# Kernel optimization log

Hardware: AMD Instinct MI355X
Metric: run time of the kernel (lower is better)

## Reference

```python
import jax, jax.numpy as jnp
import numpy as np

NUM_HEADS = 16


def setup_inputs() -> dict:
    key = jax.random.key(0)
    k1, k2, k3 = jax.random.split(key, 3)
    B, N, C = 2, 2048, 1024
    x = jax.random.normal(k1, (B, N, C), dtype=jnp.float32)
    w_qkv = jax.random.normal(k2, (3 * C, C), dtype=jnp.float32) * (C ** -0.5)
    w_proj = jax.random.normal(k3, (C, C), dtype=jnp.float32) * (C ** -0.5)
    b_proj = jnp.zeros((C,), dtype=jnp.float32)
    return {"x": x, "w_qkv": w_qkv, "w_proj": w_proj, "b_proj": b_proj}


def reference(x, w_qkv, w_proj, b_proj):
    B, N, C = x.shape
    H = NUM_HEADS
    D = C // H
    scale = 1.0 / jnp.sqrt(jnp.asarray(D, x.dtype))
    qkv = (x @ w_qkv.T).reshape(B, N, 3, H, D)
    qkv = jnp.transpose(qkv, (2, 0, 3, 1, 4))  # [3,B,H,N,D]
    q, k, v = qkv[0], qkv[1], qkv[2]
    # scaled dot-product attention with explicit score matrix [B,H,N,N]
    attn = jnp.einsum('bhnd,bhmd->bhnm', q, k) * scale
    attn = jax.nn.softmax(attn, axis=-1)
    out = jnp.einsum('bhnm,bhmd->bhnd', attn, v)
    out = jnp.transpose(out, (0, 2, 1, 3)).reshape(B, N, C)
    # output projection
    return out @ w_proj.T + b_proj
```

## Files before the change

kernel.cpp:

```cpp
#include <hip/hip_runtime.h>

typedef unsigned short u16;
typedef __attribute__((ext_vector_type(8))) short bf16x8;
typedef __attribute__((ext_vector_type(4))) float f32x4;
typedef __attribute__((ext_vector_type(16))) float f32x16;
typedef __attribute__((ext_vector_type(4))) unsigned u32x4;

#define B_ 2
#define N_ 2048
#define C_ 1024
#define H_ 16
#define D_ 64
#define M_ (B_ * N_)

#define QSCALE 0.18033688011114336f

#define EXP2R(x) __builtin_amdgcn_exp2f(x)

__device__ __forceinline__ u16 f2bf(float f) {
    union { float f; unsigned u; } x; x.f = f;
    return (u16)((x.u + 0x8000u) >> 16);
}
__device__ __forceinline__ unsigned pack2bf(float a, float b) {
    union { float f; unsigned u; } x, y; x.f = a; y.f = b;
    return __builtin_amdgcn_perm(y.u + 0x8000u, x.u + 0x8000u, 0x07060302);
}

__device__ __forceinline__ void async_copy16(const void* gsrc, void* ldst) {
    __builtin_amdgcn_global_load_lds(
        (__attribute__((address_space(1))) void*)gsrc,
        (__attribute__((address_space(3))) void*)ldst,
        16, 0, 0);
}

__global__ void cast3_kernel(const float* __restrict__ x, const float* __restrict__ wq,
                             const float* __restrict__ wp, u16* __restrict__ xo,
                             u16* __restrict__ wqo, u16* __restrict__ wpo) {
    int b = blockIdx.x;
    const float* s; u16* d;
    if (b < 4096)      { s = x;  d = xo;  }
    else if (b < 7168) { s = wq; d = wqo; b -= 4096; }
    else               { s = wp; d = wpo; b -= 7168; }
    int i = (b * 256 + threadIdx.x) * 4;
    const float4 v = *(const float4*)(s + i);
    uint2 o;
    o.x = pack2bf(v.x, v.y);
    o.y = pack2bf(v.z, v.w);
    *(uint2*)(d + i) = o;
}

template <int EPI>
__global__ __launch_bounds__(256, 3) void gemm_bt(
    const u16* __restrict__ A, const u16* __restrict__ Bm,
    int M, int Ncols, int K, int ntiles_n,
    u16* __restrict__ qo, u16* __restrict__ ko, u16* __restrict__ vt,
    const float* __restrict__ bias, float* __restrict__ out) {
    __shared__ u16 As[128 * 64];
    __shared__ u16 Bs[128 * 64];
    const int tid = threadIdx.x, lane = tid & 63, w = tid >> 6;
    const int cpx = gridDim.x >> 3;
    const int sbid = (blockIdx.x & 7) * cpx + (blockIdx.x >> 3);
    const int bx = sbid % ntiles_n, by = sbid / ntiles_n;
    const int m0 = by * 128, n0 = bx * 128;
    const int wm = w >> 1, wn = w & 1;
    const int q16 = lane >> 4, l15 = lane & 15;
    const int r0 = lane >> 3, c0 = (lane & 7) * 8;
    f32x4 acc[4][4] = {};

    for (int k0 = 0; k0 < K; k0 += 64) {
#pragma unroll
        for (int i = 0; i < 4; ++i) {
            int blk = w * 4 + i;
            int r = blk * 8 + r0;
            async_copy16(A + (size_t)(m0 + r) * K + k0 + c0, (char*)As + blk * 1024);
            async_copy16(Bm + (size_t)(n0 + r) * K + k0 + c0, (char*)Bs + blk * 1024);
        }
        __builtin_amdgcn_s_waitcnt(0);
        __syncthreads();
#pragma unroll
        for (int ks = 0; ks < 2; ++ks) {
            bf16x8 af[4], bf[4];
#pragma unroll
            for (int i = 0; i < 4; ++i) {
                af[i] = *(const bf16x8*)&As[(wm * 64 + i * 16 + l15) * 64 + ks * 32 + q16 * 8];
                bf[i] = *(const bf16x8*)&Bs[(wn * 64 + i * 16 + l15) * 64 + ks * 32 + q16 * 8];
            }
#pragma unroll
            for (int mi = 0; mi < 4; ++mi)
#pragma unroll
                for (int ni = 0; ni < 4; ++ni)
                    acc[mi][ni] = __builtin_amdgcn_mfma_f32_16x16x32_bf16(af[mi], bf[ni], acc[mi][ni], 0, 0, 0);
        }
        __syncthreads();
    }

#pragma unroll
    for (int mi = 0; mi < 4; ++mi) {
#pragma unroll
        for (int ni = 0; ni < 4; ++ni) {
            int n_g = n0 + wn * 64 + ni * 16 + l15;
            if (EPI == 0) {
                int which = n_g >> 10;
                int h = (n_g >> 6) & 15;
                int d = n_g & 63;
                int m_base = m0 + wm * 64 + mi * 16 + q16 * 4;
                int b = m_base >> 11;
                int nn0 = m_base & 2047;
                if (which == 2) {
                    uint2 pk;
                    pk.x = pack2bf(acc[mi][ni][0], acc[mi][ni][1]);
                    pk.y = pack2bf(acc[mi][ni][2], acc[mi][ni][3]);
                    *(uint2*)(vt + ((size_t)((b * H_ + h) * D_ + d) << 11) + nn0) = pk;
                } else {
                    size_t base = ((size_t)((b * H_ + h) * N_ + nn0) << 6) + d;
#pragma unroll
                    for (int r = 0; r < 4; ++r) {
                        float v = acc[mi][ni][r];
                        if (which == 0) qo[base + (size_t)r * D_] = f2bf(v * QSCALE);
                        else            ko[base + (size_t)r * D_] = f2bf(v);
                    }
                }
            } else {
#pragma unroll
                for (int r = 0; r < 4; ++r) {
                    int m_g = m0 + wm * 64 + mi * 16 + q16 * 4 + r;
                    out[(size_t)m_g * Ncols + n_g] = acc[mi][ni][r] + bias[n_g];
                }
            }
        }
    }
}

__global__ __launch_bounds__(512, 1) void attn_kernel(
    const u16* __restrict__ Q, const u16* __restrict__ K,
    const u16* __restrict__ VT, u16* __restrict__ O) {
    __shared__ u16 Ks[2][2][64 * 64];
    __shared__ u16 Vs[2][2][64 * 64];
    const int tid = threadIdx.x, lane = tid & 63, w = tid >> 6;
    const int l31 = lane & 31, hi = lane >> 5, l7 = l31 & 7;
    const int bid = blockIdx.x;
    const int bh = (bid & 7) * 4 + (bid >> 6);
    const int q0 = ((bid >> 3) & 7) * 256;
    const size_t head = (size_t)bh * N_ * D_;
    const int lr3 = lane >> 3, lc7 = lane & 7;

    auto stage = [&](int kt, int buf) {
        int key0 = kt * 128;
        int row = w * 8 + lr3;
#pragma unroll
        for (int s = 0; s < 2; ++s) {
            async_copy16(K + head + (size_t)(key0 + s * 64 + row) * D_ + (lc7 ^ lr3) * 8,
                         (char*)Ks[buf][s] + w * 1024);
            async_copy16(VT + head + (size_t)row * N_ + key0 + s * 64 + (lc7 ^ lr3) * 8,
                         (char*)Vs[buf][s] + w * 1024);
        }
    };

    bf16x8 qf[4];
#pragma unroll
    for (int ds = 0; ds < 4; ++ds)
        qf[ds] = *(const bf16x8*)(Q + head + (size_t)(q0 + w * 32 + l31) * D_ + ds * 16 + hi * 8);
    stage(0, 0);
    __builtin_amdgcn_s_waitcnt(0);
    __syncthreads();

    f32x16 o_acc[2] = {};
    float rs = 0.f;

    for (int kt = 0; kt < 16; ++kt) {
        int buf = kt & 1;
        stage((kt + 1) & 15, buf ^ 1);

#pragma unroll
        for (int s = 0; s < 2; ++s) {
#pragma unroll
            for (int kb2 = 0; kb2 < 2; ++kb2) {
                f32x16 st = {};
                __builtin_amdgcn_s_setprio(1);
#pragma unroll
                for (int ds = 0; ds < 4; ++ds) {
                    bf16x8 kf = *(const bf16x8*)&Ks[buf][s][(kb2 * 32 + l31) * 64 + ((ds * 2 + hi) ^ l7) * 8];
                    st = __builtin_amdgcn_mfma_f32_32x32x16_bf16(kf, qf[ds], st, 0, 0, 0);
                }
                __builtin_amdgcn_s_setprio(0);

                float p[16];
#pragma unroll
                for (int i = 0; i < 16; ++i) p[i] = EXP2R(st[i]);
#pragma unroll
                for (int i = 0; i < 16; ++i) rs += p[i];

                unsigned a0 = pack2bf(p[0], p[1]),   b0 = pack2bf(p[4], p[5]);
                unsigned a1 = pack2bf(p[2], p[3]),   b1 = pack2bf(p[6], p[7]);
                unsigned a2 = pack2bf(p[8], p[9]),   b2 = pack2bf(p[12], p[13]);
                unsigned a3 = pack2bf(p[10], p[11]), b3 = pack2bf(p[14], p[15]);
                asm("v_permlane32_swap_b32 %0, %1" : "+v"(a0), "+v"(b0));
                asm("v_permlane32_swap_b32 %0, %1" : "+v"(a1), "+v"(b1));
                asm("v_permlane32_swap_b32 %0, %1" : "+v"(a2), "+v"(b2));
                asm("v_permlane32_swap_b32 %0, %1" : "+v"(a3), "+v"(b3));
                union { u32x4 u; bf16x8 v; } af0, af1;
                af0.u = (u32x4){a0, a1, b0, b1};
                af1.u = (u32x4){a2, a3, b2, b3};

                __builtin_amdgcn_s_setprio(1);
#pragma unroll
                for (int db = 0; db < 2; ++db) {
                    bf16x8 vf0 = *(const bf16x8*)&Vs[buf][s][(db * 32 + l31) * 64 + ((kb2 * 4 + hi) ^ l7) * 8];
                    o_acc[db] = __builtin_amdgcn_mfma_f32_32x32x16_bf16(af0.v, vf0, o_acc[db], 0, 0, 0);
                    bf16x8 vf1 = *(const bf16x8*)&Vs[buf][s][(db * 32 + l31) * 64 + ((kb2 * 4 + 2 + hi) ^ l7) * 8];
                    o_acc[db] = __builtin_amdgcn_mfma_f32_32x32x16_bf16(af1.v, vf1, o_acc[db], 0, 0, 0);
                }
                __builtin_amdgcn_s_setprio(0);
            }
        }

        __builtin_amdgcn_s_waitcnt(0);
        __syncthreads();
    }

    rs += __shfl_xor(rs, 32);
    float rsi = 1.0f / rs;

    const int b = bh >> 4, h = bh & 15;
#pragma unroll
    for (int reg = 0; reg < 16; ++reg) {
        int qrow = (reg & 3) + 8 * (reg >> 2) + 4 * hi;
        float inv = __shfl(rsi, qrow);
        int qg = q0 + w * 32 + qrow;
#pragma unroll
        for (int db = 0; db < 2; ++db) {
            int d = db * 32 + l31;
            O[((size_t)(b * N_ + qg) << 10) + h * 64 + d] = f2bf(o_acc[db][reg] * inv);
        }
    }
}

extern "C" void kernel_launch(void* const* d_in, const int* in_sizes, int n_in,
                              void* d_out, int out_size, void* d_ws, size_t ws_size,
                              hipStream_t stream) {
    const float* x      = (const float*)d_in[0];
    const float* w_qkv  = (const float*)d_in[1];
    const float* w_proj = (const float*)d_in[2];
    const float* b_proj = (const float*)d_in[3];
    float* out = (float*)d_out;

    char* ws = (char*)d_ws;
    const size_t MB = 1024 * 1024;
    u16* x_bf     = (u16*)(ws + 0 * MB);
    u16* wqkv_bf  = (u16*)(ws + 8 * MB);
    u16* wproj_bf = (u16*)(ws + 14 * MB);
    u16* q_bf     = (u16*)(ws + 16 * MB);
    u16* k_bf     = (u16*)(ws + 24 * MB);
    u16* vt_bf    = (u16*)(ws + 32 * MB);
    u16* ao_bf    = (u16*)(ws + 40 * MB);

    cast3_kernel<<<8192, 256, 0, stream>>>(x, w_qkv, w_proj, x_bf, wqkv_bf, wproj_bf);

    gemm_bt<0><<<32 * 24, 256, 0, stream>>>(x_bf, wqkv_bf, M_, 3 * C_, C_, 24,
                                            q_bf, k_bf, vt_bf, nullptr, nullptr);

    attn_kernel<<<256, 512, 0, stream>>>(q_bf, k_bf, vt_bf, ao_bf);

    gemm_bt<1><<<32 * 8, 256, 0, stream>>>(ao_bf, wproj_bf, M_, C_, C_, 8,
                                           nullptr, nullptr, nullptr, b_proj, out);
}
```

Baseline: 181.7 us.

## Process two query tiles per wave in attention, halving waves per block

The attention kernel now runs 4 waves per block instead of 8. Each wave handles 64 query rows split into two 32-row groups, so every K and V fragment read from LDS feeds two MFMAs instead of one. The staging loop gives each wave twice as many async copies so the same tile is still loaded. The bf16 packing of probabilities also switches to the hardware v_cvt_pk_bf16_f32 instruction. In exchange, register pressure roughly doubles and fewer waves per CU are available to hide latency.

```diff
diff --git a/kernel.cpp b/kernel.cpp
--- a/kernel.cpp
+++ b/kernel.cpp
@@ -24,6 +24,11 @@
 __device__ __forceinline__ unsigned pack2bf(float a, float b) {
     union { float f; unsigned u; } x, y; x.f = a; y.f = b;
     return __builtin_amdgcn_perm(y.u + 0x8000u, x.u + 0x8000u, 0x07060302);
+}
+__device__ __forceinline__ unsigned cvtpk2bf(float a, float b) {
+    unsigned r;
+    asm("v_cvt_pk_bf16_f32 %0, %1, %2" : "=v"(r) : "v"(a), "v"(b));
+    return r;
 }
 
 __device__ __forceinline__ void async_copy16(const void* gsrc, void* ldst) {
@@ -131,7 +136,7 @@
     }
 }
 
-__global__ __launch_bounds__(512, 1) void attn_kernel(
+__global__ __launch_bounds__(256, 1) void attn_kernel(
     const u16* __restrict__ Q, const u16* __restrict__ K,
     const u16* __restrict__ VT, u16* __restrict__ O) {
     __shared__ u16 Ks[2][2][64 * 64];
@@ -146,26 +151,32 @@
 
     auto stage = [&](int kt, int buf) {
         int key0 = kt * 128;
-        int row = w * 8 + lr3;
-#pragma unroll
-        for (int s = 0; s < 2; ++s) {
-            async_copy16(K + head + (size_t)(key0 + s * 64 + row) * D_ + (lc7 ^ lr3) * 8,
-                         (char*)Ks[buf][s] + w * 1024);
-            async_copy16(VT + head + (size_t)row * N_ + key0 + s * 64 + (lc7 ^ lr3) * 8,
-                         (char*)Vs[buf][s] + w * 1024);
-        }
+#pragma unroll
+        for (int s = 0; s < 2; ++s)
+#pragma unroll
+            for (int i = 0; i < 2; ++i) {
+                int c = w * 2 + i;
+                int row = c * 8 + lr3;
+                async_copy16(K + head + (size_t)(key0 + s * 64 + row) * D_ + (lc7 ^ lr3) * 8,
+                             (char*)Ks[buf][s] + c * 1024);
+                async_copy16(VT + head + (size_t)row * N_ + key0 + s * 64 + (lc7 ^ lr3) * 8,
+                             (char*)Vs[buf][s] + c * 1024);
+            }
     };
 
-    bf16x8 qf[4];
-#pragma unroll
-    for (int ds = 0; ds < 4; ++ds)
-        qf[ds] = *(const bf16x8*)(Q + head + (size_t)(q0 + w * 32 + l31) * D_ + ds * 16 + hi * 8);
+    bf16x8 qf[2][4];
+#pragma unroll
+    for (int qg = 0; qg < 2; ++qg)
+#pragma unroll
+        for (int ds = 0; ds < 4; ++ds)
+            qf[qg][ds] = *(const bf16x8*)(Q + head +
+                (size_t)(q0 + w * 64 + qg * 32 + l31) * D_ + ds * 16 + hi * 8);
     stage(0, 0);
     __builtin_amdgcn_s_waitcnt(0);
     __syncthreads();
 
-    f32x16 o_acc[2] = {};
-    float rs = 0.f;
+    f32x16 o_acc[2][2] = {};
+    float rs[2] = {0.f, 0.f};
 
     for (int kt = 0; kt < 16; ++kt) {
         int buf = kt & 1;
@@ -175,40 +186,49 @@
         for (int s = 0; s < 2; ++s) {
 #pragma unroll
             for (int kb2 = 0; kb2 < 2; ++kb2) {
-                f32x16 st = {};
+                bf16x8 kf[4];
+#pragma unroll
+                for (int ds = 0; ds < 4; ++ds)
+                    kf[ds] = *(const bf16x8*)&Ks[buf][s][(kb2 * 32 + l31) * 64 + ((ds * 2 + hi) ^ l7) * 8];
+                f32x16 st0 = {}, st1 = {};
                 __builtin_amdgcn_s_setprio(1);
 #pragma unroll
                 for (int ds = 0; ds < 4; ++ds) {
-                    bf16x8 kf = *(const bf16x8*)&Ks[buf][s][(kb2 * 32 + l31) * 64 + ((ds * 2 + hi) ^ l7) * 8];
-                    st = __builtin_amdgcn_mfma_f32_32x32x16_bf16(kf, qf[ds], st, 0, 0, 0);
+                    st0 = __builtin_amdgcn_mfma_f32_32x32x16_bf16(kf[ds], qf[0][ds], st0, 0, 0, 0);
+                    st1 = __builtin_amdgcn_mfma_f32_32x32x16_bf16(kf[ds], qf[1][ds], st1, 0, 0, 0);
                 }
                 __builtin_amdgcn_s_setprio(0);
 
-                float p[16];
-#pragma unroll
-                for (int i = 0; i < 16; ++i) p[i] = EXP2R(st[i]);
-#pragma unroll
-                for (int i = 0; i < 16; ++i) rs += p[i];
-
-                unsigned a0 = pack2bf(p[0], p[1]),   b0 = pack2bf(p[4], p[5]);
-                unsigned a1 = pack2bf(p[2], p[3]),   b1 = pack2bf(p[6], p[7]);
-                unsigned a2 = pack2bf(p[8], p[9]),   b2 = pack2bf(p[12], p[13]);
-                unsigned a3 = pack2bf(p[10], p[11]), b3 = pack2bf(p[14], p[15]);
-                asm("v_permlane32_swap_b32 %0, %1" : "+v"(a0), "+v"(b0));
-                asm("v_permlane32_swap_b32 %0, %1" : "+v"(a1), "+v"(b1));
-                asm("v_permlane32_swap_b32 %0, %1" : "+v"(a2), "+v"(b2));
-                asm("v_permlane32_swap_b32 %0, %1" : "+v"(a3), "+v"(b3));
-                union { u32x4 u; bf16x8 v; } af0, af1;
-                af0.u = (u32x4){a0, a1, b0, b1};
-                af1.u = (u32x4){a2, a3, b2, b3};
+                union { u32x4 u; bf16x8 v; } af0[2], af1[2];
+#pragma unroll
+                for (int qg = 0; qg < 2; ++qg) {
+                    const f32x16& st = qg ? st1 : st0;
+                    float p[16];
+#pragma unroll
+                    for (int i = 0; i < 16; ++i) p[i] = EXP2R(st[i]);
+#pragma unroll
+                    for (int i = 0; i < 16; ++i) rs[qg] += p[i];
+                    unsigned a0 = cvtpk2bf(p[0], p[1]),   b0 = cvtpk2bf(p[4], p[5]);
+                    unsigned a1 = cvtpk2bf(p[2], p[3]),   b1 = cvtpk2bf(p[6], p[7]);
+                    unsigned a2 = cvtpk2bf(p[8], p[9]),   b2 = cvtpk2bf(p[12], p[13]);
+                    unsigned a3 = cvtpk2bf(p[10], p[11]), b3 = cvtpk2bf(p[14], p[15]);
+                    asm("v_permlane32_swap_b32 %0, %1" : "+v"(a0), "+v"(b0));
+                    asm("v_permlane32_swap_b32 %0, %1" : "+v"(a1), "+v"(b1));
+                    asm("v_permlane32_swap_b32 %0, %1" : "+v"(a2), "+v"(b2));
+                    asm("v_permlane32_swap_b32 %0, %1" : "+v"(a3), "+v"(b3));
+                    af0[qg].u = (u32x4){a0, a1, b0, b1};
+                    af1[qg].u = (u32x4){a2, a3, b2, b3};
+                }
 
                 __builtin_amdgcn_s_setprio(1);
 #pragma unroll
                 for (int db = 0; db < 2; ++db) {
                     bf16x8 vf0 = *(const bf16x8*)&Vs[buf][s][(db * 32 + l31) * 64 + ((kb2 * 4 + hi) ^ l7) * 8];
-                    o_acc[db] = __builtin_amdgcn_mfma_f32_32x32x16_bf16(af0.v, vf0, o_acc[db], 0, 0, 0);
+                    o_acc[0][db] = __builtin_amdgcn_mfma_f32_32x32x16_bf16(af0[0].v, vf0, o_acc[0][db], 0, 0, 0);
+                    o_acc[1][db] = __builtin_amdgcn_mfma_f32_32x32x16_bf16(af0[1].v, vf0, o_acc[1][db], 0, 0, 0);
                     bf16x8 vf1 = *(const bf16x8*)&Vs[buf][s][(db * 32 + l31) * 64 + ((kb2 * 4 + 2 + hi) ^ l7) * 8];
-                    o_acc[db] = __builtin_amdgcn_mfma_f32_32x32x16_bf16(af1.v, vf1, o_acc[db], 0, 0, 0);
+                    o_acc[0][db] = __builtin_amdgcn_mfma_f32_32x32x16_bf16(af1[0].v, vf1, o_acc[0][db], 0, 0, 0);
+                    o_acc[1][db] = __builtin_amdgcn_mfma_f32_32x32x16_bf16(af1[1].v, vf1, o_acc[1][db], 0, 0, 0);
                 }
                 __builtin_amdgcn_s_setprio(0);
             }
@@ -218,19 +238,21 @@
         __syncthreads();
     }
 
-    rs += __shfl_xor(rs, 32);
-    float rsi = 1.0f / rs;
-
     const int b = bh >> 4, h = bh & 15;
 #pragma unroll
-    for (int reg = 0; reg < 16; ++reg) {
-        int qrow = (reg & 3) + 8 * (reg >> 2) + 4 * hi;
-        float inv = __shfl(rsi, qrow);
-        int qg = q0 + w * 32 + qrow;
-#pragma unroll
-        for (int db = 0; db < 2; ++db) {
-            int d = db * 32 + l31;
-            O[((size_t)(b * N_ + qg) << 10) + h * 64 + d] = f2bf(o_acc[db][reg] * inv);
+    for (int qg = 0; qg < 2; ++qg) {
+        rs[qg] += __shfl_xor(rs[qg], 32);
+        float rsi = 1.0f / rs[qg];
+#pragma unroll
+        for (int reg = 0; reg < 16; ++reg) {
+            int qrow = (reg & 3) + 8 * (reg >> 2) + 4 * hi;
+            float inv = __shfl(rsi, qrow);
+            int qg_g = q0 + w * 64 + qg * 32 + qrow;
+#pragma unroll
+            for (int db = 0; db < 2; ++db) {
+                int d = db * 32 + l31;
+                O[((size_t)(b * N_ + qg_g) << 10) + h * 64 + d] = f2bf(o_acc[qg][db][reg] * inv);
+            }
         }
     }
 }
@@ -259,7 +281,7 @@
     gemm_bt<0><<<32 * 24, 256, 0, stream>>>(x_bf, wqkv_bf, M_, 3 * C_, C_, 24,
                                             q_bf, k_bf, vt_bf, nullptr, nullptr);
 
-    attn_kernel<<<256, 512, 0, stream>>>(q_bf, k_bf, vt_bf, ao_bf);
+    attn_kernel<<<256, 256, 0, stream>>>(q_bf, k_bf, vt_bf, ao_bf);
 
     gemm_bt<1><<<32 * 8, 256, 0, stream>>>(ao_bf, wproj_bf, M_, C_, C_, 8,
                                            nullptr, nullptr, nullptr, b_proj, out);
```

Result: slower. 193.6 us (+6.6%).

## Split attention into smaller blocks with batched LDS loads and hardware bf16 packing

Applied to the files above, without the earlier changes.

The attention kernel moves from 256 blocks of 512 threads (256 queries each, 128-key tiles) to 512 blocks of 256 threads (128 queries each, 64-key tiles), with two blocks per CU. All K and V fragments for a tile are loaded from LDS up front, and the two score MFMA chains are interleaved. The manual bf16 rounding/pack is replaced by v_cvt_pk_bf16_f32. The goal is better occupancy and latency hiding, at the cost of twice as many tile iterations and barriers, plus more register pressure from the preloaded fragments.

```diff
diff --git a/kernel.cpp b/kernel.cpp
--- a/kernel.cpp
+++ b/kernel.cpp
@@ -24,6 +24,11 @@
 __device__ __forceinline__ unsigned pack2bf(float a, float b) {
     union { float f; unsigned u; } x, y; x.f = a; y.f = b;
     return __builtin_amdgcn_perm(y.u + 0x8000u, x.u + 0x8000u, 0x07060302);
+}
+__device__ __forceinline__ unsigned cvtpk2bf(float a, float b) {
+    unsigned r;
+    asm("v_cvt_pk_bf16_f32 %0, %1, %2" : "=v"(r) : "v"(a), "v"(b));
+    return r;
 }
 
 __device__ __forceinline__ void async_copy16(const void* gsrc, void* ldst) {
@@ -131,28 +136,29 @@
     }
 }
 
-__global__ __launch_bounds__(512, 1) void attn_kernel(
+__global__ __launch_bounds__(256, 2) void attn_kernel(
     const u16* __restrict__ Q, const u16* __restrict__ K,
     const u16* __restrict__ VT, u16* __restrict__ O) {
-    __shared__ u16 Ks[2][2][64 * 64];
-    __shared__ u16 Vs[2][2][64 * 64];
+    __shared__ u16 Ks[2][64 * 64];
+    __shared__ u16 Vs[2][64 * 64];
     const int tid = threadIdx.x, lane = tid & 63, w = tid >> 6;
     const int l31 = lane & 31, hi = lane >> 5, l7 = l31 & 7;
     const int bid = blockIdx.x;
-    const int bh = (bid & 7) * 4 + (bid >> 6);
-    const int q0 = ((bid >> 3) & 7) * 256;
+    const int bh = (bid & 7) * 4 + (bid >> 7);
+    const int q0 = ((bid >> 3) & 15) * 128;
     const size_t head = (size_t)bh * N_ * D_;
     const int lr3 = lane >> 3, lc7 = lane & 7;
 
     auto stage = [&](int kt, int buf) {
-        int key0 = kt * 128;
-        int row = w * 8 + lr3;
-#pragma unroll
-        for (int s = 0; s < 2; ++s) {
-            async_copy16(K + head + (size_t)(key0 + s * 64 + row) * D_ + (lc7 ^ lr3) * 8,
-                         (char*)Ks[buf][s] + w * 1024);
-            async_copy16(VT + head + (size_t)row * N_ + key0 + s * 64 + (lc7 ^ lr3) * 8,
-                         (char*)Vs[buf][s] + w * 1024);
+        int key0 = kt * 64;
+#pragma unroll
+        for (int i = 0; i < 2; ++i) {
+            int c = w * 2 + i;
+            int row = c * 8 + lr3;
+            async_copy16(K + head + (size_t)(key0 + row) * D_ + (lc7 ^ lr3) * 8,
+                         (char*)Ks[buf] + c * 1024);
+            async_copy16(VT + head + (size_t)row * N_ + key0 + (lc7 ^ lr3) * 8,
+                         (char*)Vs[buf] + c * 1024);
         }
     };
 
@@ -167,52 +173,68 @@
     f32x16 o_acc[2] = {};
     float rs = 0.f;
 
-    for (int kt = 0; kt < 16; ++kt) {
+    for (int kt = 0; kt < 32; ++kt) {
         int buf = kt & 1;
-        stage((kt + 1) & 15, buf ^ 1);
-
-#pragma unroll
-        for (int s = 0; s < 2; ++s) {
-#pragma unroll
-            for (int kb2 = 0; kb2 < 2; ++kb2) {
-                f32x16 st = {};
-                __builtin_amdgcn_s_setprio(1);
-#pragma unroll
-                for (int ds = 0; ds < 4; ++ds) {
-                    bf16x8 kf = *(const bf16x8*)&Ks[buf][s][(kb2 * 32 + l31) * 64 + ((ds * 2 + hi) ^ l7) * 8];
-                    st = __builtin_amdgcn_mfma_f32_32x32x16_bf16(kf, qf[ds], st, 0, 0, 0);
-                }
-                __builtin_amdgcn_s_setprio(0);
-
-                float p[16];
-#pragma unroll
-                for (int i = 0; i < 16; ++i) p[i] = EXP2R(st[i]);
-#pragma unroll
-                for (int i = 0; i < 16; ++i) rs += p[i];
-
-                unsigned a0 = pack2bf(p[0], p[1]),   b0 = pack2bf(p[4], p[5]);
-                unsigned a1 = pack2bf(p[2], p[3]),   b1 = pack2bf(p[6], p[7]);
-                unsigned a2 = pack2bf(p[8], p[9]),   b2 = pack2bf(p[12], p[13]);
-                unsigned a3 = pack2bf(p[10], p[11]), b3 = pack2bf(p[14], p[15]);
-                asm("v_permlane32_swap_b32 %0, %1" : "+v"(a0), "+v"(b0));
-                asm("v_permlane32_swap_b32 %0, %1" : "+v"(a1), "+v"(b1));
-                asm("v_permlane32_swap_b32 %0, %1" : "+v"(a2), "+v"(b2));
-                asm("v_permlane32_swap_b32 %0, %1" : "+v"(a3), "+v"(b3));
-                union { u32x4 u; bf16x8 v; } af0, af1;
-                af0.u = (u32x4){a0, a1, b0, b1};
-                af1.u = (u32x4){a2, a3, b2, b3};
-
-                __builtin_amdgcn_s_setprio(1);
-#pragma unroll
-                for (int db = 0; db < 2; ++db) {
-                    bf16x8 vf0 = *(const bf16x8*)&Vs[buf][s][(db * 32 + l31) * 64 + ((kb2 * 4 + hi) ^ l7) * 8];
-                    o_acc[db] = __builtin_amdgcn_mfma_f32_32x32x16_bf16(af0.v, vf0, o_acc[db], 0, 0, 0);
-                    bf16x8 vf1 = *(const bf16x8*)&Vs[buf][s][(db * 32 + l31) * 64 + ((kb2 * 4 + 2 + hi) ^ l7) * 8];
-                    o_acc[db] = __builtin_amdgcn_mfma_f32_32x32x16_bf16(af1.v, vf1, o_acc[db], 0, 0, 0);
-                }
-                __builtin_amdgcn_s_setprio(0);
-            }
-        }
+        stage((kt + 1) & 31, buf ^ 1);
+
+        bf16x8 kf[2][4];
+        bf16x8 vlo[2][2];
+        bf16x8 vhi[2][2];
+#pragma unroll
+        for (int kb2 = 0; kb2 < 2; ++kb2) {
+#pragma unroll
+            for (int ds = 0; ds < 4; ++ds)
+                kf[kb2][ds] = *(const bf16x8*)&Ks[buf][(kb2 * 32 + l31) * 64 + ((ds * 2 + hi) ^ l7) * 8];
+#pragma unroll
+            for (int db = 0; db < 2; ++db) {
+                vlo[kb2][db] = *(const bf16x8*)&Vs[buf][(db * 32 + l31) * 64 + ((kb2 * 4 + hi) ^ l7) * 8];
+                vhi[kb2][db] = *(const bf16x8*)&Vs[buf][(db * 32 + l31) * 64 + ((kb2 * 4 + 2 + hi) ^ l7) * 8];
+            }
+        }
+
+        f32x16 st0 = {}, st1 = {};
+        __builtin_amdgcn_s_setprio(1);
+#pragma unroll
+        for (int ds = 0; ds < 4; ++ds) {
+            st0 = __builtin_amdgcn_mfma_f32_32x32x16_bf16(kf[0][ds], qf[ds], st0, 0, 0, 0);
+            st1 = __builtin_amdgcn_mfma_f32_32x32x16_bf16(kf[1][ds], qf[ds], st1, 0, 0, 0);
+        }
+        __builtin_amdgcn_s_setprio(0);
+
+        union { u32x4 u; bf16x8 v; } af0[2], af1[2];
+#pragma unroll
+        for (int kb2 = 0; kb2 < 2; ++kb2) {
+            float p[16];
+            if (kb2 == 0) {
+#pragma unroll
+                for (int i = 0; i < 16; ++i) p[i] = EXP2R(st0[i]);
+            } else {
+#pragma unroll
+                for (int i = 0; i < 16; ++i) p[i] = EXP2R(st1[i]);
+            }
+#pragma unroll
+            for (int i = 0; i < 16; ++i) rs += p[i];
+            unsigned a0 = cvtpk2bf(p[0], p[1]),   b0 = cvtpk2bf(p[4], p[5]);
+            unsigned a1 = cvtpk2bf(p[2], p[3]),   b1 = cvtpk2bf(p[6], p[7]);
+            unsigned a2 = cvtpk2bf(p[8], p[9]),   b2 = cvtpk2bf(p[12], p[13]);
+            unsigned a3 = cvtpk2bf(p[10], p[11]), b3 = cvtpk2bf(p[14], p[15]);
+            asm("v_permlane32_swap_b32 %0, %1" : "+v"(a0), "+v"(b0));
+            asm("v_permlane32_swap_b32 %0, %1" : "+v"(a1), "+v"(b1));
+            asm("v_permlane32_swap_b32 %0, %1" : "+v"(a2), "+v"(b2));
+            asm("v_permlane32_swap_b32 %0, %1" : "+v"(a3), "+v"(b3));
+            af0[kb2].u = (u32x4){a0, a1, b0, b1};
+            af1[kb2].u = (u32x4){a2, a3, b2, b3};
+        }
+
+        __builtin_amdgcn_s_setprio(1);
+#pragma unroll
+        for (int kb2 = 0; kb2 < 2; ++kb2) {
+            o_acc[0] = __builtin_amdgcn_mfma_f32_32x32x16_bf16(af0[kb2].v, vlo[kb2][0], o_acc[0], 0, 0, 0);
+            o_acc[1] = __builtin_amdgcn_mfma_f32_32x32x16_bf16(af0[kb2].v, vlo[kb2][1], o_acc[1], 0, 0, 0);
+            o_acc[0] = __builtin_amdgcn_mfma_f32_32x32x16_bf16(af1[kb2].v, vhi[kb2][0], o_acc[0], 0, 0, 0);
+            o_acc[1] = __builtin_amdgcn_mfma_f32_32x32x16_bf16(af1[kb2].v, vhi[kb2][1], o_acc[1], 0, 0, 0);
+        }
+        __builtin_amdgcn_s_setprio(0);
 
         __builtin_amdgcn_s_waitcnt(0);
         __syncthreads();
@@ -220,7 +242,6 @@
 
     rs += __shfl_xor(rs, 32);
     float rsi = 1.0f / rs;
-
     const int b = bh >> 4, h = bh & 15;
 #pragma unroll
     for (int reg = 0; reg < 16; ++reg) {
@@ -259,7 +280,7 @@
     gemm_bt<0><<<32 * 24, 256, 0, stream>>>(x_bf, wqkv_bf, M_, 3 * C_, C_, 24,
                                             q_bf, k_bf, vt_bf, nullptr, nullptr);
 
-    attn_kernel<<<256, 512, 0, stream>>>(q_bf, k_bf, vt_bf, ao_bf);
+    attn_kernel<<<512, 256, 0, stream>>>(q_bf, k_bf, vt_bf, ao_bf);
 
     gemm_bt<1><<<32 * 8, 256, 0, stream>>>(ao_bf, wproj_bf, M_, C_, C_, 8,
                                            nullptr, nullptr, nullptr, b_proj, out);
```

New measurement: 184.8 us. Within noise of the previous version (+1.7%).
